# Kernel optimization log

Hardware: AMD Instinct MI355X
Metric: run time of the kernel (lower is better)

Reference implementation:

```python
import jax, jax.numpy as jnp
import numpy as np
from jax.ops import segment_sum

NEG_SLOPE = 0.2
N0, N1, N2, N3 = 100000, 300000, 150000, 50000
DIN, DMID = 64, 128


def setup_inputs() -> dict:
    key = jax.random.key(0)
    ks = jax.random.split(key, 16)
    g = lambda k, shp, fan_in: jax.random.normal(k, shp, dtype=jnp.float32) * (1.0 / np.sqrt(fan_in))
    return {
        "x_0": jax.random.normal(ks[0], (N0, DIN), dtype=jnp.float32),
        "x_1": jax.random.normal(ks[1], (N1, DIN), dtype=jnp.float32),
        "x_2": jax.random.normal(ks[2], (N2, DIN), dtype=jnp.float32),
        "x_3": jax.random.normal(ks[3], (N3, DIN), dtype=jnp.float32),
        "x_4": jax.random.normal(ks[4], (10000, DIN), dtype=jnp.float32),
        # COO indices: row 0 = destination (row of sparse matrix), row 1 = source (column)
        "adj0_idx": jax.random.randint(ks[5], (2, 800000), 0, N0),
        "adj3_idx": jax.random.randint(ks[6], (2, 800000), 0, N3),
        "inc01_t": jax.random.randint(ks[7], (600000,), 0, N0),   # rows of incidence_0_1 (0-cells)
        "inc01_s": jax.random.randint(ks[8], (600000,), 0, N1),   # cols (1-cells)
        "inc23_t": jax.random.randint(ks[9], (200000,), 0, N2),   # rows of incidence_2_3 (2-cells)
        "inc23_s": jax.random.randint(ks[10], (200000,), 0, N3),  # cols (3-cells)
        "W_hbs0": g(ks[11], (DIN, DMID), DIN),
        "W_hbs3": g(ks[12], (DIN, DMID), DIN),
        "W_s01": g(ks[13], (DIN, DMID), DIN),   # HBNS source weight: x_1 -> target-rank (0) messages
        "W_t23": g(ks[14], (DIN, DMID), DIN),   # HBNS target weight: x_2 -> source-rank (3) messages
        "fc0_W": g(ks[15], (DMID, DMID), DMID),
        "fc0_b": jnp.zeros((DMID,), dtype=jnp.float32),
        "fc3_W": g(jax.random.fold_in(key, 100), (DMID, DMID), DMID),
        "fc3_b": jnp.zeros((DMID,), dtype=jnp.float32),
    }


def _spmm(msg, dst, src, n_out):
    # out[i] = sum_{(i,j) in nnz} msg[j]  == sparse_matrix @ msg
    return segment_sum(msg[src], dst, num_segments=n_out)


def reference(x_0, x_1, x_2, x_3, x_4, adj0_idx, adj3_idx, inc01_t, inc01_s,
              inc23_t, inc23_s, W_hbs0, W_hbs3, W_s01, W_t23,
              fc0_W, fc0_b, fc3_W, fc3_b):
    lrelu = lambda v: jax.nn.leaky_relu(v, NEG_SLOPE)
    # HBS within-rank propagation: A @ (x W)
    x_0_to_0 = _spmm(x_0 @ W_hbs0, adj0_idx[0], adj0_idx[1], x_0.shape[0])
    x_3_to_3 = _spmm(x_3 @ W_hbs3, adj3_idx[0], adj3_idx[1], x_3.shape[0])
    # HBNS cross-rank propagation
    # message on target rank 0: incidence_0_1 @ (x_1 W_s)
    x_1_to_0 = _spmm(x_1 @ W_s01, inc01_t, inc01_s, x_0.shape[0])
    # message on source rank 3: incidence_2_3^T @ (x_2 W_t)
    x_2_to_3 = _spmm(x_2 @ W_t23, inc23_s, inc23_t, x_3.shape[0])
    # sum aggregation + FC + LeakyReLU
    x_0_new = lrelu((x_0_to_0 + x_1_to_0) @ fc0_W.T + fc0_b)
    x_3_new = lrelu((x_2_to_3 + x_3_to_3) @ fc3_W.T + fc3_b)
    return (x_0_new, x_1, x_2, x_3_new, x_4)
```

## Files before the change

kernel.cpp:

```cpp
#include <hip/hip_runtime.h>

#define NEG_SLOPE 0.2f


__global__ __launch_bounds__(256) void hist_kernel(const int* __restrict__ dst,
                                                   int* __restrict__ counts,
                                                   int E, int base) {
    int i = blockIdx.x * 256 + threadIdx.x;
    int stride = gridDim.x * 256;
    for (; i < E; i += stride) atomicAdd(&counts[base + dst[i]], 1);
}

__global__ __launch_bounds__(256) void chunk_sum(const int* __restrict__ counts,
                                                 int* __restrict__ bsum, int NT) {
    __shared__ int red[256];
    int base = blockIdx.x * 2048;
    int t = threadIdx.x;
    int s = 0;
#pragma unroll
    for (int j = 0; j < 8; ++j) {
        int idx = base + j * 256 + t;
        if (idx < NT) s += counts[idx];
    }
    red[t] = s;
    __syncthreads();
    for (int off = 128; off > 0; off >>= 1) {
        if (t < off) red[t] += red[t + off];
        __syncthreads();
    }
    if (t == 0) bsum[blockIdx.x] = red[0];
}

__global__ __launch_bounds__(256) void scan_bsum(const int* __restrict__ bsum,
                                                 int* __restrict__ bbase, int nb) {
    __shared__ int sh[256];
    int t = threadIdx.x;
    int v = (t < nb) ? bsum[t] : 0;
    sh[t] = v;
    __syncthreads();
    for (int off = 1; off < 256; off <<= 1) {
        int add = (t >= off) ? sh[t - off] : 0;
        __syncthreads();
        sh[t] += add;
        __syncthreads();
    }
    if (t < nb) bbase[t] = sh[t] - v;
}

__global__ __launch_bounds__(256) void chunk_scan(const int* __restrict__ counts,
                                                  const int* __restrict__ bbase,
                                                  int* __restrict__ offsets,
                                                  int* __restrict__ cursors,
                                                  int NT, int E_total) {
    __shared__ int tsum[256];
    int t = threadIdx.x;
    int base = blockIdx.x * 2048 + t * 8;
    int v[8];
    int s = 0;
#pragma unroll
    for (int j = 0; j < 8; ++j) {
        int idx = base + j;
        v[j] = (idx < NT) ? counts[idx] : 0;
        s += v[j];
    }
    tsum[t] = s;
    __syncthreads();
    for (int off = 1; off < 256; off <<= 1) {
        int add = (t >= off) ? tsum[t - off] : 0;
        __syncthreads();
        tsum[t] += add;
        __syncthreads();
    }
    int run = bbase[blockIdx.x] + tsum[t] - s;
#pragma unroll
    for (int j = 0; j < 8; ++j) {
        int idx = base + j;
        if (idx < NT) { offsets[idx] = run; cursors[idx] = run; }
        run += v[j];
    }
    if (blockIdx.x == 0 && t == 0) offsets[NT] = E_total;
}

__global__ __launch_bounds__(256) void fill_kernel(const int* __restrict__ dst,
                                                   const int* __restrict__ src,
                                                   int* __restrict__ cursors,
                                                   int* __restrict__ edge_src,
                                                   int E, int base) {
    int i = blockIdx.x * 256 + threadIdx.x;
    int stride = gridDim.x * 256;
    for (; i < E; i += stride) {
        int d = dst[i];
        int pos = atomicAdd(&cursors[base + d], 1);
        edge_src[pos] = src[i];
    }
}

__global__ __launch_bounds__(256) void gather_kernel(const int* __restrict__ offsets,
                                                     const int* __restrict__ edge_src,
                                                     const float* __restrict__ x0,
                                                     const float* __restrict__ x1,
                                                     const float* __restrict__ x2,
                                                     const float* __restrict__ x3,
                                                     float* __restrict__ agg0,
                                                     float* __restrict__ agg3,
                                                     int n0, int n3) {
    const int NT = 2 * n0 + 2 * n3;
    int row = blockIdx.x * 4 + (threadIdx.x >> 6);
    int lane = threadIdx.x & 63;
    if (row >= NT) return;
    const float* xs;
    float* out;
    if (row < n0) {
        xs = x0; out = &agg0[(size_t)row * 128 + lane];
    } else if (row < 2 * n0) {
        xs = x1; out = &agg0[(size_t)(row - n0) * 128 + 64 + lane];
    } else if (row < 2 * n0 + n3) {
        xs = x3; out = &agg3[(size_t)(row - 2 * n0) * 128 + lane];
    } else {
        xs = x2; out = &agg3[(size_t)(row - 2 * n0 - n3) * 128 + 64 + lane];
    }
    int beg = offsets[row], end = offsets[row + 1];
    float acc = 0.f;
    int k = beg;
    for (; k + 1 < end; k += 2) {
        int s0 = edge_src[k];
        int s1 = edge_src[k + 1];
        float a = xs[(size_t)s0 * 64 + lane];
        float b = xs[(size_t)s1 * 64 + lane];
        acc += a;
        acc += b;
    }
    if (k < end) acc += xs[(size_t)edge_src[k] * 64 + lane];
    *out = acc;
}

__global__ __launch_bounds__(256) void combine_w(const float* __restrict__ Wtop,
                                                 const float* __restrict__ Wbot,
                                                 const float* __restrict__ F,
                                                 float* __restrict__ WC) {
    int i = blockIdx.x * 256 + threadIdx.x;
    int k = i >> 7;
    int c = i & 127;
    const float* wrow = (k < 64) ? &Wtop[(size_t)k * 128] : &Wbot[(size_t)(k - 64) * 128];
    const float* frow = &F[(size_t)c * 128];
    float s = 0.f;
#pragma unroll 8
    for (int j = 0; j < 128; j += 4) {
        float4 w = *(const float4*)&wrow[j];
        float4 f = *(const float4*)&frow[j];
        s = fmaf(w.x, f.x, s);
        s = fmaf(w.y, f.y, s);
        s = fmaf(w.z, f.z, s);
        s = fmaf(w.w, f.w, s);
    }
    WC[(size_t)k * 128 + c] = s;
}

__global__ __launch_bounds__(256) void fc_lrelu(const float* __restrict__ A,
                                                const float* __restrict__ WC,
                                                const float* __restrict__ bias,
                                                float* __restrict__ Y, int n) {
    __shared__ float WS[64][128];
    __shared__ float XS[64][68];
    const int t = threadIdx.x;
    const int row0 = blockIdx.x * 64;
    const int c = (t & 31) * 4;
    const int rbase = (t >> 5) * 8;
    float acc[8][4];
#pragma unroll
    for (int i = 0; i < 8; ++i)
#pragma unroll
        for (int j = 0; j < 4; ++j) acc[i][j] = 0.f;

    for (int p = 0; p < 2; ++p) {
        __syncthreads();
        const float4* Wp4 = (const float4*)(WC + (size_t)p * 64 * 128);
        float4* WS4 = (float4*)&WS[0][0];
        for (int i = t; i < 2048; i += 256) WS4[i] = Wp4[i];
        for (int i = t; i < 64 * 16; i += 256) {
            int r = i >> 4, c4 = i & 15;
            float4 v = make_float4(0.f, 0.f, 0.f, 0.f);
            if (row0 + r < n)
                v = *(const float4*)&A[(size_t)(row0 + r) * 128 + p * 64 + c4 * 4];
            *(float4*)&XS[r][c4 * 4] = v;
        }
        __syncthreads();

#pragma unroll 4
        for (int k = 0; k < 64; k += 4) {
            float4 w[4];
            w[0] = *(const float4*)&WS[k + 0][c];
            w[1] = *(const float4*)&WS[k + 1][c];
            w[2] = *(const float4*)&WS[k + 2][c];
            w[3] = *(const float4*)&WS[k + 3][c];
#pragma unroll
            for (int i = 0; i < 8; ++i) {
                float4 x = *(const float4*)&XS[rbase + i][k];
                float xs[4] = {x.x, x.y, x.z, x.w};
#pragma unroll
                for (int kk = 0; kk < 4; ++kk) {
                    acc[i][0] = fmaf(xs[kk], w[kk].x, acc[i][0]);
                    acc[i][1] = fmaf(xs[kk], w[kk].y, acc[i][1]);
                    acc[i][2] = fmaf(xs[kk], w[kk].z, acc[i][2]);
                    acc[i][3] = fmaf(xs[kk], w[kk].w, acc[i][3]);
                }
            }
        }
    }

    float4 b = *(const float4*)&bias[c];
    float bs[4] = {b.x, b.y, b.z, b.w};
#pragma unroll
    for (int i = 0; i < 8; ++i) {
        int r = row0 + rbase + i;
        if (r < n) {
            float o[4];
#pragma unroll
            for (int j = 0; j < 4; ++j) {
                float v = acc[i][j] + bs[j];
                o[j] = v > 0.f ? v : NEG_SLOPE * v;
            }
            *(float4*)&Y[(size_t)r * 128 + c] = make_float4(o[0], o[1], o[2], o[3]);
        }
    }
}

extern "C" void kernel_launch(void* const* d_in, const int* in_sizes, int n_in,
                              void* d_out, int out_size, void* d_ws, size_t ws_size,
                              hipStream_t stream) {
    const float* x0 = (const float*)d_in[0];
    const float* x1 = (const float*)d_in[1];
    const float* x2 = (const float*)d_in[2];
    const float* x3 = (const float*)d_in[3];
    const float* x4 = (const float*)d_in[4];
    const int* adj0 = (const int*)d_in[5];
    const int* adj3 = (const int*)d_in[6];
    const int* inc01_t = (const int*)d_in[7];
    const int* inc01_s = (const int*)d_in[8];
    const int* inc23_t = (const int*)d_in[9];
    const int* inc23_s = (const int*)d_in[10];
    const float* W_hbs0 = (const float*)d_in[11];
    const float* W_hbs3 = (const float*)d_in[12];
    const float* W_s01 = (const float*)d_in[13];
    const float* W_t23 = (const float*)d_in[14];
    const float* fc0_W = (const float*)d_in[15];
    const float* fc0_b = (const float*)d_in[16];
    const float* fc3_W = (const float*)d_in[17];
    const float* fc3_b = (const float*)d_in[18];

    const int n0 = in_sizes[0] / 64, n1 = in_sizes[1] / 64;
    const int n2 = in_sizes[2] / 64, n3 = in_sizes[3] / 64, n4 = in_sizes[4] / 64;
    const int E0 = in_sizes[5] / 2, E3 = in_sizes[6] / 2;
    const int E01 = in_sizes[7], E23 = in_sizes[9];
    const int NT = 2 * n0 + 2 * n3;
    const int E_total = E0 + E01 + E3 + E23;
    const int nb = (NT + 2047) / 2048;

    float* ws = (float*)d_ws;
    size_t off = 0;
    float* agg0 = ws + off; off += (size_t)n0 * 128;
    float* agg3 = ws + off; off += (size_t)n3 * 128;
    float* wc0 = ws + off;  off += 16384;
    float* wc3 = ws + off;  off += 16384;
    int* counts = (int*)(ws + off);   off += NT;
    int* offsets = (int*)(ws + off);  off += NT + 1;
    int* cursors = (int*)(ws + off);  off += NT;
    int* bsum = (int*)(ws + off);     off += 256;
    int* bbase = (int*)(ws + off);    off += 256;
    int* edge_src = (int*)(ws + off); off += E_total;

    float* out = (float*)d_out;
    float* o_x0 = out;
    float* o_x1 = o_x0 + (size_t)n0 * 128;
    float* o_x2 = o_x1 + (size_t)n1 * 64;
    float* o_x3 = o_x2 + (size_t)n2 * 64;
    float* o_x4 = o_x3 + (size_t)n3 * 128;

    hipMemsetAsync(counts, 0, (size_t)NT * sizeof(int), stream);
    auto gblocks = [](int E) { return (E + 255) / 256; };
    hist_kernel<<<gblocks(E0), 256, 0, stream>>>(adj0, counts, E0, 0);
    hist_kernel<<<gblocks(E01), 256, 0, stream>>>(inc01_t, counts, E01, n0);
    hist_kernel<<<gblocks(E3), 256, 0, stream>>>(adj3, counts, E3, 2 * n0);
    hist_kernel<<<gblocks(E23), 256, 0, stream>>>(inc23_s, counts, E23, 2 * n0 + n3);

    chunk_sum<<<nb, 256, 0, stream>>>(counts, bsum, NT);
    scan_bsum<<<1, 256, 0, stream>>>(bsum, bbase, nb);
    chunk_scan<<<nb, 256, 0, stream>>>(counts, bbase, offsets, cursors, NT, E_total);

    fill_kernel<<<gblocks(E0), 256, 0, stream>>>(adj0, adj0 + E0, cursors, edge_src, E0, 0);
    fill_kernel<<<gblocks(E01), 256, 0, stream>>>(inc01_t, inc01_s, cursors, edge_src, E01, n0);
    fill_kernel<<<gblocks(E3), 256, 0, stream>>>(adj3, adj3 + E3, cursors, edge_src, E3, 2 * n0);
    fill_kernel<<<gblocks(E23), 256, 0, stream>>>(inc23_s, inc23_t, cursors, edge_src, E23, 2 * n0 + n3);

    gather_kernel<<<(NT + 3) / 4, 256, 0, stream>>>(offsets, edge_src, x0, x1, x2, x3,
                                                    agg0, agg3, n0, n3);

    combine_w<<<64, 256, 0, stream>>>(W_hbs0, W_s01, fc0_W, wc0);
    combine_w<<<64, 256, 0, stream>>>(W_hbs3, W_t23, fc3_W, wc3);
    fc_lrelu<<<(n0 + 63) / 64, 256, 0, stream>>>(agg0, wc0, fc0_b, o_x0, n0);
    fc_lrelu<<<(n3 + 63) / 64, 256, 0, stream>>>(agg3, wc3, fc3_b, o_x3, n3);

    hipMemcpyAsync(o_x1, x1, (size_t)n1 * 64 * sizeof(float), hipMemcpyDeviceToDevice, stream);
    hipMemcpyAsync(o_x2, x2, (size_t)n2 * 64 * sizeof(float), hipMemcpyDeviceToDevice, stream);
    hipMemcpyAsync(o_x4, x4, (size_t)n4 * 64 * sizeof(float), hipMemcpyDeviceToDevice, stream);
}
```

Measured before the change: 871.6 us.

## Merge histogram, fill, combine and copy launches; vectorize gather with float4 edge groups

Folds the four histogram launches and the four CSR fill launches into one kernel each, the two weight-combine launches into one, and replaces three device memcpys with a single copy kernel. This cuts launch and tail overhead. The gather kernel now has each wavefront split into four 16-lane groups, each group reading a whole float4 row for a different edge, with a cross-group shuffle reduction at the end. That gives wider loads and more independent gathers in flight, at the cost of extra shuffle work and a 3/4 idle tail on low-degree rows.

```diff
diff --git a/kernel.cpp b/kernel.cpp
--- a/kernel.cpp
+++ b/kernel.cpp
@@ -3,12 +3,24 @@
 #define NEG_SLOPE 0.2f
 
 
-__global__ __launch_bounds__(256) void hist_kernel(const int* __restrict__ dst,
-                                                   int* __restrict__ counts,
-                                                   int E, int base) {
+__global__ __launch_bounds__(256) void hist_all(const int* __restrict__ ad0,
+                                                const int* __restrict__ d1,
+                                                const int* __restrict__ ad3,
+                                                const int* __restrict__ d2,
+                                                int E0, int E01, int E3, int E23,
+                                                int n0, int n3,
+                                                int* __restrict__ counts) {
+    int T = E0 + E01 + E3 + E23;
     int i = blockIdx.x * 256 + threadIdx.x;
     int stride = gridDim.x * 256;
-    for (; i < E; i += stride) atomicAdd(&counts[base + dst[i]], 1);
+    for (; i < T; i += stride) {
+        int j = i, d, base;
+        if (j < E0) { d = ad0[j]; base = 0; }
+        else if ((j -= E0) < E01) { d = d1[j]; base = n0; }
+        else if ((j -= E01) < E3) { d = ad3[j]; base = 2 * n0; }
+        else { j -= E3; d = d2[j]; base = 2 * n0 + n3; }
+        atomicAdd(&counts[base + d], 1);
+    }
 }
 
 __global__ __launch_bounds__(256) void chunk_sum(const int* __restrict__ counts,
@@ -81,17 +93,29 @@
     if (blockIdx.x == 0 && t == 0) offsets[NT] = E_total;
 }
 
-__global__ __launch_bounds__(256) void fill_kernel(const int* __restrict__ dst,
-                                                   const int* __restrict__ src,
-                                                   int* __restrict__ cursors,
-                                                   int* __restrict__ edge_src,
-                                                   int E, int base) {
+__global__ __launch_bounds__(256) void fill_all(const int* __restrict__ ad0,
+                                                const int* __restrict__ as0,
+                                                const int* __restrict__ d1,
+                                                const int* __restrict__ s1,
+                                                const int* __restrict__ ad3,
+                                                const int* __restrict__ as3,
+                                                const int* __restrict__ d2,
+                                                const int* __restrict__ s2,
+                                                int E0, int E01, int E3, int E23,
+                                                int n0, int n3,
+                                                int* __restrict__ cursors,
+                                                int* __restrict__ edge_src) {
+    int T = E0 + E01 + E3 + E23;
     int i = blockIdx.x * 256 + threadIdx.x;
     int stride = gridDim.x * 256;
-    for (; i < E; i += stride) {
-        int d = dst[i];
+    for (; i < T; i += stride) {
+        int j = i, d, s, base;
+        if (j < E0) { d = ad0[j]; s = as0[j]; base = 0; }
+        else if ((j -= E0) < E01) { d = d1[j]; s = s1[j]; base = n0; }
+        else if ((j -= E01) < E3) { d = ad3[j]; s = as3[j]; base = 2 * n0; }
+        else { j -= E3; d = d2[j]; s = s2[j]; base = 2 * n0 + n3; }
         int pos = atomicAdd(&cursors[base + d], 1);
-        edge_src[pos] = src[i];
+        edge_src[pos] = s;
     }
 }
 
@@ -106,39 +130,64 @@
                                                      int n0, int n3) {
     const int NT = 2 * n0 + 2 * n3;
     int row = blockIdx.x * 4 + (threadIdx.x >> 6);
+    if (row >= NT) return;
     int lane = threadIdx.x & 63;
-    if (row >= NT) return;
+    int g = lane >> 4;
+    int c4 = (lane & 15) * 4;
     const float* xs;
-    float* out;
-    if (row < n0) {
-        xs = x0; out = &agg0[(size_t)row * 128 + lane];
-    } else if (row < 2 * n0) {
-        xs = x1; out = &agg0[(size_t)(row - n0) * 128 + 64 + lane];
-    } else if (row < 2 * n0 + n3) {
-        xs = x3; out = &agg3[(size_t)(row - 2 * n0) * 128 + lane];
-    } else {
-        xs = x2; out = &agg3[(size_t)(row - 2 * n0 - n3) * 128 + 64 + lane];
-    }
+    float* outp;
+    if (row < n0)               { xs = x0; outp = &agg0[(size_t)row * 128]; }
+    else if (row < 2 * n0)      { xs = x1; outp = &agg0[(size_t)(row - n0) * 128 + 64]; }
+    else if (row < 2 * n0 + n3) { xs = x3; outp = &agg3[(size_t)(row - 2 * n0) * 128]; }
+    else                        { xs = x2; outp = &agg3[(size_t)(row - 2 * n0 - n3) * 128 + 64]; }
+
     int beg = offsets[row], end = offsets[row + 1];
-    float acc = 0.f;
+    float4 acc = make_float4(0.f, 0.f, 0.f, 0.f);
     int k = beg;
-    for (; k + 1 < end; k += 2) {
-        int s0 = edge_src[k];
-        int s1 = edge_src[k + 1];
-        float a = xs[(size_t)s0 * 64 + lane];
-        float b = xs[(size_t)s1 * 64 + lane];
-        acc += a;
-        acc += b;
-    }
-    if (k < end) acc += xs[(size_t)edge_src[k] * 64 + lane];
-    *out = acc;
-}
-
-__global__ __launch_bounds__(256) void combine_w(const float* __restrict__ Wtop,
-                                                 const float* __restrict__ Wbot,
-                                                 const float* __restrict__ F,
-                                                 float* __restrict__ WC) {
-    int i = blockIdx.x * 256 + threadIdx.x;
+    for (; k + 8 <= end; k += 8) {
+        int i0 = edge_src[k + g];
+        int i1 = edge_src[k + 4 + g];
+        float4 a = *(const float4*)&xs[(size_t)i0 * 64 + c4];
+        float4 b = *(const float4*)&xs[(size_t)i1 * 64 + c4];
+        acc.x += a.x; acc.y += a.y; acc.z += a.z; acc.w += a.w;
+        acc.x += b.x; acc.y += b.y; acc.z += b.z; acc.w += b.w;
+    }
+    int rem = end - k;
+    if (g < rem) {
+        int i0 = edge_src[k + g];
+        float4 a = *(const float4*)&xs[(size_t)i0 * 64 + c4];
+        acc.x += a.x; acc.y += a.y; acc.z += a.z; acc.w += a.w;
+    }
+    if (rem > 4 && g < rem - 4) {
+        int i1 = edge_src[k + 4 + g];
+        float4 b = *(const float4*)&xs[(size_t)i1 * 64 + c4];
+        acc.x += b.x; acc.y += b.y; acc.z += b.z; acc.w += b.w;
+    }
+#pragma unroll
+    for (int d = 16; d < 64; d <<= 1) {
+        acc.x += __shfl_xor(acc.x, d, 64);
+        acc.y += __shfl_xor(acc.y, d, 64);
+        acc.z += __shfl_xor(acc.z, d, 64);
+        acc.w += __shfl_xor(acc.w, d, 64);
+    }
+    if (g == 0) *(float4*)&outp[c4] = acc;
+}
+
+__global__ __launch_bounds__(256) void combine_w2(const float* __restrict__ Wtop0,
+                                                  const float* __restrict__ Wbot0,
+                                                  const float* __restrict__ F0,
+                                                  float* __restrict__ WC0,
+                                                  const float* __restrict__ Wtop3,
+                                                  const float* __restrict__ Wbot3,
+                                                  const float* __restrict__ F3,
+                                                  float* __restrict__ WC3) {
+    int gi = blockIdx.x * 256 + threadIdx.x;
+    int which = gi >> 14;
+    int i = gi & 16383;
+    const float* Wtop = which ? Wtop3 : Wtop0;
+    const float* Wbot = which ? Wbot3 : Wbot0;
+    const float* F = which ? F3 : F0;
+    float* WC = which ? WC3 : WC0;
     int k = i >> 7;
     int c = i & 127;
     const float* wrow = (k < 64) ? &Wtop[(size_t)k * 128] : &Wbot[(size_t)(k - 64) * 128];
@@ -222,6 +271,20 @@
             }
             *(float4*)&Y[(size_t)r * 128 + c] = make_float4(o[0], o[1], o[2], o[3]);
         }
+    }
+}
+
+__global__ __launch_bounds__(256) void copy_all(const float4* __restrict__ s1, float4* __restrict__ o1, int m1,
+                                                const float4* __restrict__ s2, float4* __restrict__ o2, int m2,
+                                                const float4* __restrict__ s4, float4* __restrict__ o4, int m4) {
+    int total = m1 + m2 + m4;
+    int i = blockIdx.x * 256 + threadIdx.x;
+    int stride = gridDim.x * 256;
+    for (; i < total; i += stride) {
+        int j = i;
+        if (j < m1) { o1[j] = s1[j]; }
+        else if ((j -= m1) < m2) { o2[j] = s2[j]; }
+        else { j -= m2; o4[j] = s4[j]; }
     }
 }
 
@@ -277,30 +340,24 @@
     float* o_x4 = o_x3 + (size_t)n3 * 128;
 
     hipMemsetAsync(counts, 0, (size_t)NT * sizeof(int), stream);
-    auto gblocks = [](int E) { return (E + 255) / 256; };
-    hist_kernel<<<gblocks(E0), 256, 0, stream>>>(adj0, counts, E0, 0);
-    hist_kernel<<<gblocks(E01), 256, 0, stream>>>(inc01_t, counts, E01, n0);
-    hist_kernel<<<gblocks(E3), 256, 0, stream>>>(adj3, counts, E3, 2 * n0);
-    hist_kernel<<<gblocks(E23), 256, 0, stream>>>(inc23_s, counts, E23, 2 * n0 + n3);
-
+    hist_all<<<(E_total + 255) / 256, 256, 0, stream>>>(
+        adj0, inc01_t, adj3, inc23_s, E0, E01, E3, E23, n0, n3, counts);
     chunk_sum<<<nb, 256, 0, stream>>>(counts, bsum, NT);
     scan_bsum<<<1, 256, 0, stream>>>(bsum, bbase, nb);
     chunk_scan<<<nb, 256, 0, stream>>>(counts, bbase, offsets, cursors, NT, E_total);
-
-    fill_kernel<<<gblocks(E0), 256, 0, stream>>>(adj0, adj0 + E0, cursors, edge_src, E0, 0);
-    fill_kernel<<<gblocks(E01), 256, 0, stream>>>(inc01_t, inc01_s, cursors, edge_src, E01, n0);
-    fill_kernel<<<gblocks(E3), 256, 0, stream>>>(adj3, adj3 + E3, cursors, edge_src, E3, 2 * n0);
-    fill_kernel<<<gblocks(E23), 256, 0, stream>>>(inc23_s, inc23_t, cursors, edge_src, E23, 2 * n0 + n3);
+    fill_all<<<(E_total + 255) / 256, 256, 0, stream>>>(
+        adj0, adj0 + E0, inc01_t, inc01_s, adj3, adj3 + E3, inc23_s, inc23_t,
+        E0, E01, E3, E23, n0, n3, cursors, edge_src);
 
     gather_kernel<<<(NT + 3) / 4, 256, 0, stream>>>(offsets, edge_src, x0, x1, x2, x3,
                                                     agg0, agg3, n0, n3);
 
-    combine_w<<<64, 256, 0, stream>>>(W_hbs0, W_s01, fc0_W, wc0);
-    combine_w<<<64, 256, 0, stream>>>(W_hbs3, W_t23, fc3_W, wc3);
+    combine_w2<<<128, 256, 0, stream>>>(W_hbs0, W_s01, fc0_W, wc0,
+                                        W_hbs3, W_t23, fc3_W, wc3);
     fc_lrelu<<<(n0 + 63) / 64, 256, 0, stream>>>(agg0, wc0, fc0_b, o_x0, n0);
     fc_lrelu<<<(n3 + 63) / 64, 256, 0, stream>>>(agg3, wc3, fc3_b, o_x3, n3);
 
-    hipMemcpyAsync(o_x1, x1, (size_t)n1 * 64 * sizeof(float), hipMemcpyDeviceToDevice, stream);
-    hipMemcpyAsync(o_x2, x2, (size_t)n2 * 64 * sizeof(float), hipMemcpyDeviceToDevice, stream);
-    hipMemcpyAsync(o_x4, x4, (size_t)n4 * 64 * sizeof(float), hipMemcpyDeviceToDevice, stream);
-}
+    copy_all<<<8192, 256, 0, stream>>>((const float4*)x1, (float4*)o_x1, n1 * 16,
+                                       (const float4*)x2, (float4*)o_x2, n2 * 16,
+                                       (const float4*)x4, (float4*)o_x4, n4 * 16);
+}
```

New measurement: 800.7 us. -8.1%, faster.
